# Performance work log

Hardware: AMD Instinct MI355X
Metric: run time of the kernel (lower is better)

Reference implementation:

```python
import jax, jax.numpy as jnp
import numpy as np

B, DV, W, H = 64, 2048, 14, 14
DQ, DA, G, DH, NC = 2400, 1200, 2, 1200, 3000


def setup_inputs() -> dict:
    key = jax.random.key(0)
    ks = jax.random.split(key, 14)
    s = lambda k, shp, scale=0.02: jax.random.normal(k, shp, dtype=jnp.float32) * scale
    return {
        "input_q": jax.random.normal(ks[0], (B, DQ), dtype=jnp.float32),
        "input_v": jax.random.normal(ks[1], (B, DV, W, H), dtype=jnp.float32),
        "Wv_att": s(ks[2], (DA, DV)),
        "bv_att": s(ks[3], (DA,)),
        "Wq_att": s(ks[4], (DA, DQ)),
        "bq_att": s(ks[5], (DA,)),
        "Watt": s(ks[6], (G, DA)),
        "batt": s(ks[7], (G,)),
        "Wv_fus": s(ks[8], (G, DH, DV)),
        "bv_fus": s(ks[9], (G, DH)),
        "Wq_fus": s(ks[10], (G * DH, DQ)),
        "bq_fus": s(ks[11], (G * DH,)),
        "Wc": s(ks[12], (NC, G * DH)),
        "bc": s(ks[13], (NC,)),
    }


def reference(input_q, input_v, Wv_att, bv_att, Wq_att, bq_att, Watt, batt,
              Wv_fus, bv_fus, Wq_fus, bq_fus, Wc, bc):
    b, dv, w, h = input_v.shape
    n = w * h  # spatial positions

    # --- attention branch (eval mode: dropout = identity) ---
    # 1x1 conv == per-position linear over channels; activation_v = tanh
    xv = jnp.tanh(jnp.einsum('bchw,dc->bdhw', input_v, Wv_att) + bv_att[None, :, None, None])
    xv = xv.reshape(b, -1, n).transpose(0, 2, 1)               # [B, WH, DA]
    # question projection; activation_q = tanh
    xq = jnp.tanh(input_q @ Wq_att.T + bq_att)                 # [B, DA]
    # MLB Hadamard fusion + activation_mm = tanh
    xatt = jnp.tanh(xv * xq[:, None, :])                       # [B, WH, DA]
    # glimpse scores: 1x1 conv over dim_mm channels
    wgt = jnp.einsum('bnd,gd->bgn', xatt, Watt) + batt[None, :, None]  # [B, G, WH]
    att = jax.nn.softmax(wgt, axis=-1)                         # softmax over WH per glimpse

    # weighted sum of ORIGINAL features per glimpse
    v_flat = input_v.reshape(b, dv, n)                         # [B, DV, WH]
    v_att = jnp.einsum('bgn,bdn->bgd', att, v_flat)            # [B, G, DV]

    # --- glimpse fusion + classification ---
    v_fus = jnp.tanh(jnp.einsum('bgd,ghd->bgh', v_att, Wv_fus) + bv_fus)  # [B, G, DH]
    v_fus = v_fus.reshape(b, -1)                               # [B, G*DH] (concat over glimpses)
    q_fus = jnp.tanh(input_q @ Wq_fus.T + bq_fus)              # [B, G*DH]
    x = (v_fus * q_fus) @ Wc.T + bc                            # [B, NC]
    return (x, wgt)
```

## Files before the change

kernel.cpp:

```cpp
#include <hip/hip_runtime.h>
#include <hip/hip_fp16.h>

typedef _Float16 half8 __attribute__((ext_vector_type(8)));
typedef float f32x4 __attribute__((ext_vector_type(4)));

__device__ __forceinline__ float tanh_fast(float x) {
  float e = __expf(2.0f * x);
  return 1.0f - 2.0f / (e + 1.0f);
}

__device__ __forceinline__ void gload16(const _Float16* g, _Float16* l) {
  __builtin_amdgcn_global_load_lds((const __attribute__((address_space(1))) void*)g,
                                   (__attribute__((address_space(3))) void*)l,
                                   16, 0, 0);
}

__global__ __launch_bounds__(256) void k_transpose_v(const float* __restrict__ in,
                                                     _Float16* __restrict__ out) {
  __shared__ float t[64][65];
  int b = blockIdx.z;
  int c0 = blockIdx.y * 64;
  int p0 = blockIdx.x * 64;
  int tid = threadIdx.x;
  int pl = tid & 63;
  #pragma unroll
  for (int s = 0; s < 16; ++s) {
    int cl = (tid >> 6) + s * 4;
    int p = p0 + pl;
    t[cl][pl] = (p < 196) ? in[((size_t)b * 2048 + (c0 + cl)) * 196 + p] : 0.0f;
  }
  __syncthreads();
  int c8 = (tid & 7) * 8;
  #pragma unroll
  for (int s = 0; s < 2; ++s) {
    int p = p0 + (tid >> 3) + s * 32;
    if (p < 196) {
      half8 v;
      #pragma unroll
      for (int j = 0; j < 8; ++j) v[j] = (_Float16)t[c8 + j][(tid >> 3) + s * 32];
      *(half8*)(out + ((size_t)b * 196 + p) * 2048 + c0 + c8) = v;
    }
  }
}

__global__ __launch_bounds__(256) void k_prep(const float* __restrict__ W,
                                              _Float16* __restrict__ Wh,
                                              const float* __restrict__ batt,
                                              float* __restrict__ wgt) {
  int i = blockIdx.x * 256 + threadIdx.x;
  int n = i >> 11;
  Wh[i] = (n < 1200) ? (_Float16)W[i] : (_Float16)0.0f;
  if (i < 25088) wgt[i] = batt[(i / 196) & 1];
}

__global__ __launch_bounds__(512, 2) void k_gemm1(const _Float16* __restrict__ A,
                                                  const _Float16* __restrict__ B,
                                                  const float* __restrict__ bias,
                                                  const float* __restrict__ xq,
                                                  const float* __restrict__ Watt,
                                                  float* __restrict__ wgt) {
  __shared__ __align__(16) _Float16 AS[2][256 * 64];
  __shared__ __align__(16) _Float16 BS[2][256 * 64];
  int tid = threadIdx.x;
  int n0 = blockIdx.x * 256;
  int m0 = blockIdx.y * 256;
  int lane = tid & 63;
  int wave = tid >> 6;
  int wm = (wave >> 2) * 128;
  int wn = (wave & 3) * 64;
  int fr = lane & 15;
  int fq = lane >> 4;

  const _Float16* ap[4];
  const _Float16* bp[4];
  int ldso[4];
  #pragma unroll
  for (int i = 0; i < 4; ++i) {
    int g = i * 512 + tid;
    int r = g >> 3, c = g & 7;
    ap[i] = A + (size_t)(m0 + r) * 2048 + ((c ^ (r & 7)) << 3);
    bp[i] = B + (size_t)(n0 + r) * 2048 + ((c ^ (r & 7)) << 3);
    ldso[i] = (i * 512 + (tid & ~63)) << 3;
  }

  f32x4 acc[8][4];
  #pragma unroll
  for (int i = 0; i < 8; ++i)
    #pragma unroll
    for (int j = 0; j < 4; ++j) acc[i][j] = (f32x4){0.f, 0.f, 0.f, 0.f};

  auto stage = [&](int buf, int k0) {
    #pragma unroll
    for (int i = 0; i < 4; ++i) gload16(ap[i] + k0, &AS[buf][ldso[i]]);
    #pragma unroll
    for (int i = 0; i < 4; ++i) gload16(bp[i] + k0, &BS[buf][ldso[i]]);
  };

  auto compute = [&](int buf) {
    half8 a[4][2], b[2][2];
    #pragma unroll
    for (int mh = 0; mh < 2; ++mh) {
      #pragma unroll
      for (int mt = 0; mt < 4; ++mt)
        #pragma unroll
        for (int kk = 0; kk < 2; ++kk) {
          int row = wm + mh * 64 + mt * 16 + fr;
          int c = kk * 4 + fq;
          a[mt][kk] = *(const half8*)(&AS[buf][row * 64 + ((c ^ (row & 7)) << 3)]);
        }
      #pragma unroll
      for (int nh = 0; nh < 2; ++nh) {
        #pragma unroll
        for (int nt = 0; nt < 2; ++nt)
          #pragma unroll
          for (int kk = 0; kk < 2; ++kk) {
            int row = wn + nh * 32 + nt * 16 + fr;
            int c = kk * 4 + fq;
            b[nt][kk] = *(const half8*)(&BS[buf][row * 64 + ((c ^ (row & 7)) << 3)]);
          }
        __builtin_amdgcn_s_setprio(1);
        #pragma unroll
        for (int mt = 0; mt < 4; ++mt)
          #pragma unroll
          for (int nt = 0; nt < 2; ++nt)
            #pragma unroll
            for (int kk = 0; kk < 2; ++kk)
              acc[mh * 4 + mt][nh * 2 + nt] = __builtin_amdgcn_mfma_f32_16x16x32_f16(
                  a[mt][kk], b[nt][kk], acc[mh * 4 + mt][nh * 2 + nt], 0, 0, 0);
        __builtin_amdgcn_s_setprio(0);
      }
    }
  };

  stage(0, 0);
  stage(1, 64);
  for (int t = 0; t < 32; ++t) {
    int cur = t & 1;
    if (t < 31) asm volatile("s_waitcnt vmcnt(8)" ::: "memory");
    else        asm volatile("s_waitcnt vmcnt(0)" ::: "memory");
    __builtin_amdgcn_s_barrier();
    asm volatile("" ::: "memory");
    compute(cur);
    asm volatile("" ::: "memory");
    __builtin_amdgcn_s_barrier();
    if (t < 30) stage(cur, (t + 2) * 64);
  }

  float s0[32], s1[32];
  #pragma unroll
  for (int i = 0; i < 32; ++i) { s0[i] = 0.f; s1[i] = 0.f; }

  #pragma unroll
  for (int nf = 0; nf < 4; ++nf) {
    int col = n0 + wn + (nf >> 1) * 32 + (nf & 1) * 16 + fr;
    bool ok = col < 1200;
    float bcol = ok ? bias[col] : 0.f;
    float wa0 = ok ? Watt[col] : 0.f;
    float wa1 = ok ? Watt[1200 + col] : 0.f;
    int bprev = -1;
    float xqv = 0.f;
    #pragma unroll
    for (int mf = 0; mf < 8; ++mf) {
      #pragma unroll
      for (int r = 0; r < 4; ++r) {
        int row = m0 + wm + (mf >> 2) * 64 + (mf & 3) * 16 + fq * 4 + r;
        int b = row / 196;
        if (b != bprev) { bprev = b; xqv = ok ? xq[b * 1200 + col] : 0.f; }
        float xv = tanh_fast(acc[mf][nf][r] + bcol);
        float xa = tanh_fast(xv * xqv);
        s0[mf * 4 + r] += xa * wa0;
        s1[mf * 4 + r] += xa * wa1;
      }
    }
  }
  #pragma unroll
  for (int i = 0; i < 32; ++i) {
    #pragma unroll
    for (int off = 8; off > 0; off >>= 1) {
      s0[i] += __shfl_down(s0[i], off);
      s1[i] += __shfl_down(s1[i], off);
    }
  }
  if (fr == 0) {
    #pragma unroll
    for (int i = 0; i < 32; ++i) {
      int row = m0 + wm + ((i >> 2) >> 2) * 64 + ((i >> 2) & 3) * 16 + fq * 4 + (i & 3);
      int b = row / 196;
      int p = row - b * 196;
      atomicAdd(&wgt[(b * 2 + 0) * 196 + p], s0[i]);
      atomicAdd(&wgt[(b * 2 + 1) * 196 + p], s1[i]);
    }
  }
}

__global__ __launch_bounds__(256) void k_vatt(const _Float16* __restrict__ Vt,
                                              const float* __restrict__ wgt,
                                              float* __restrict__ v_att) {
  __shared__ float a0s[196], a1s[196];
  int b = blockIdx.y;
  int tid = threadIdx.x;
  int wv = tid >> 6, lane = tid & 63;
  if (wv < 2) {
    const float* wr = wgt + ((size_t)b * 2 + wv) * 196;
    float v[4];
    #pragma unroll
    for (int i = 0; i < 4; ++i) {
      int n = lane + i * 64;
      v[i] = (n < 196) ? wr[n] : -1e30f;
    }
    float mx = fmaxf(fmaxf(v[0], v[1]), fmaxf(v[2], v[3]));
    #pragma unroll
    for (int off = 32; off > 0; off >>= 1) mx = fmaxf(mx, __shfl_xor(mx, off));
    float s = 0.f;
    #pragma unroll
    for (int i = 0; i < 4; ++i) {
      int n = lane + i * 64;
      float e = (n < 196) ? __expf(v[i] - mx) : 0.f;
      v[i] = e;
      s += e;
    }
    #pragma unroll
    for (int off = 32; off > 0; off >>= 1) s += __shfl_xor(s, off);
    float inv = 1.f / s;
    float* dst = wv ? a1s : a0s;
    #pragma unroll
    for (int i = 0; i < 4; ++i) {
      int n = lane + i * 64;
      if (n < 196) dst[n] = v[i] * inv;
    }
  }
  __syncthreads();
  int d = blockIdx.x * 256 + tid;
  const _Float16* vp = Vt + (size_t)b * 196 * 2048 + d;
  float s0 = 0.f, s1 = 0.f;
  for (int n = 0; n < 196; ++n) {
    float v = (float)vp[(size_t)n * 2048];
    s0 += a0s[n] * v;
    s1 += a1s[n] * v;
  }
  v_att[((size_t)b * 2 + 0) * 2048 + d] = s0;
  v_att[((size_t)b * 2 + 1) * 2048 + d] = s1;
}

__global__ __launch_bounds__(256) void k_skinnyQ(const float* __restrict__ q,
                                                 const float* __restrict__ Wa,
                                                 const float* __restrict__ Wf,
                                                 int S, float* __restrict__ P) {
  __shared__ __align__(16) float As[32][64];
  __shared__ __align__(16) float Ws2[32][64];
  int tid = threadIdx.x;
  int x = blockIdx.x;
  int s = blockIdx.y;
  bool f = x >= 19;
  const float* W = f ? Wf : Wa;
  int nt0 = f ? (x - 19) * 64 : x * 64;
  int N = f ? 2400 : 1200;
  int colBase = f ? 1200 : 0;
  const int K = 2400;
  int tiles = K >> 5;
  int t0 = (s * tiles) / S;
  int t1 = ((s + 1) * tiles) / S;
  int tx = tid & 15, ty = tid >> 4;
  int lm = tid >> 2;
  int lk = (tid & 3) * 8;
  const float* Ab = q + (size_t)lm * K;
  int ng = nt0 + lm;
  const float* Wb = W + (size_t)ng * K;
  bool wok = ng < N;
  float acc[4][4] = {};
  for (int t = t0; t < t1; ++t) {
    int k0 = t * 32;
    __syncthreads();
    #pragma unroll
    for (int j = 0; j < 8; ++j) As[lk + j][lm] = Ab[k0 + lk + j];
    #pragma unroll
    for (int j = 0; j < 8; ++j) Ws2[lk + j][lm] = wok ? Wb[k0 + lk + j] : 0.0f;
    __syncthreads();
    #pragma unroll
    for (int kk = 0; kk < 32; ++kk) {
      f32x4 a = *(const f32x4*)&As[kk][ty * 4];
      f32x4 wv = *(const f32x4*)&Ws2[kk][tx * 4];
      #pragma unroll
      for (int i = 0; i < 4; ++i)
        #pragma unroll
        for (int j = 0; j < 4; ++j) acc[i][j] += a[i] * wv[j];
    }
  }
  #pragma unroll
  for (int i = 0; i < 4; ++i) {
    int m = ty * 4 + i;
    #pragma unroll
    for (int j = 0; j < 4; ++j) {
      int nl = nt0 + tx * 4 + j;
      if (nl < N) P[((size_t)s * 64 + m) * 3600 + colBase + nl] = acc[i][j];
    }
  }
}

__global__ __launch_bounds__(256) void k_combineQ(const float* __restrict__ P, int S,
                                                  const float* __restrict__ bq_att,
                                                  const float* __restrict__ bq_fus,
                                                  float* __restrict__ xq,
                                                  float* __restrict__ q_fus) {
  int i = blockIdx.x * 256 + threadIdx.x;
  if (i >= 230400) return;
  int row = i / 3600, col = i % 3600;
  float sum = 0.f;
  for (int ss = 0; ss < S; ++ss) sum += P[(size_t)ss * 230400 + i];
  if (col < 1200) xq[row * 1200 + col] = tanh_fast(sum + bq_att[col]);
  else            q_fus[row * 2400 + col - 1200] = tanh_fast(sum + bq_fus[col - 1200]);
}

__global__ __launch_bounds__(256) void k_skinny(const float* __restrict__ A1,
                                                const float* __restrict__ A2,
                                                int lda, int strideAz,
                                                const float* __restrict__ W, long strideWz,
                                                int N, int K, int S,
                                                float* __restrict__ P, int ldp, int colOffZ) {
  __shared__ __align__(16) float As[32][64];
  __shared__ __align__(16) float Ws2[32][64];
  int tid = threadIdx.x;
  int z = blockIdx.z;
  int s = blockIdx.y;
  int nt0 = blockIdx.x * 64;
  int tiles = K >> 5;
  int t0 = (s * tiles) / S;
  int t1 = ((s + 1) * tiles) / S;
  int tx = tid & 15, ty = tid >> 4;
  int lm = tid >> 2;
  int lk = (tid & 3) * 8;
  const float* Ab = A1 + (size_t)z * strideAz + (size_t)lm * lda;
  const float* A2b = A2 ? (A2 + (size_t)z * strideAz + (size_t)lm * lda) : nullptr;
  int ng = nt0 + lm;
  const float* Wb = W + (size_t)z * strideWz + (size_t)ng * K;
  bool wok = ng < N;
  float acc[4][4] = {};
  for (int t = t0; t < t1; ++t) {
    int k0 = t * 32;
    __syncthreads();
    #pragma unroll
    for (int j = 0; j < 8; ++j) {
      float v = Ab[k0 + lk + j];
      if (A2b) v *= A2b[k0 + lk + j];
      As[lk + j][lm] = v;
    }
    #pragma unroll
    for (int j = 0; j < 8; ++j) Ws2[lk + j][lm] = wok ? Wb[k0 + lk + j] : 0.0f;
    __syncthreads();
    #pragma unroll
    for (int kk = 0; kk < 32; ++kk) {
      f32x4 a = *(const f32x4*)&As[kk][ty * 4];
      f32x4 wv = *(const f32x4*)&Ws2[kk][tx * 4];
      #pragma unroll
      for (int i = 0; i < 4; ++i)
        #pragma unroll
        for (int j = 0; j < 4; ++j) acc[i][j] += a[i] * wv[j];
    }
  }
  #pragma unroll
  for (int i = 0; i < 4; ++i) {
    int m = ty * 4 + i;
    #pragma unroll
    for (int j = 0; j < 4; ++j) {
      int nl = nt0 + tx * 4 + j;
      if (nl < N) P[((size_t)s * 64 + m) * ldp + z * colOffZ + nl] = acc[i][j];
    }
  }
}

__global__ __launch_bounds__(256) void k_combineVh(const float* __restrict__ P, int S,
                                                   const float* __restrict__ bv_fus,
                                                   const float* __restrict__ q_fus,
                                                   float* __restrict__ h) {
  int i = blockIdx.x * 256 + threadIdx.x;
  if (i >= 153600) return;
  int col = i % 2400;
  float sum = bv_fus[col];
  for (int ss = 0; ss < S; ++ss) sum += P[(size_t)ss * 153600 + i];
  h[i] = tanh_fast(sum) * q_fus[i];
}

__global__ __launch_bounds__(256) void k_combine(const float* __restrict__ P, int S, int ldp,
                                                 const float* __restrict__ bias,
                                                 float* __restrict__ out, int total) {
  int i = blockIdx.x * 256 + threadIdx.x;
  if (i >= total) return;
  float sum = bias[i % ldp];
  for (int ss = 0; ss < S; ++ss) sum += P[(size_t)ss * total + i];
  out[i] = sum;
}

extern "C" void kernel_launch(void* const* d_in, const int* in_sizes, int n_in,
                              void* d_out, int out_size, void* d_ws, size_t ws_size,
                              hipStream_t stream) {
  const float* input_q = (const float*)d_in[0];
  const float* input_v = (const float*)d_in[1];
  const float* Wv_att  = (const float*)d_in[2];
  const float* bv_att  = (const float*)d_in[3];
  const float* Wq_att  = (const float*)d_in[4];
  const float* bq_att  = (const float*)d_in[5];
  const float* Watt    = (const float*)d_in[6];
  const float* batt    = (const float*)d_in[7];
  const float* Wv_fus  = (const float*)d_in[8];
  const float* bv_fus  = (const float*)d_in[9];
  const float* Wq_fus  = (const float*)d_in[10];
  const float* bq_fus  = (const float*)d_in[11];
  const float* Wc      = (const float*)d_in[12];
  const float* bc      = (const float*)d_in[13];
  float* out = (float*)d_out;

  char* ws = (char*)d_ws;
  _Float16* Vt   = (_Float16*)ws; ws += 51380224;
  _Float16* Wh   = (_Float16*)ws; ws += 5242880;
  float* xq      = (float*)ws;    ws += 307200;
  float* v_att   = (float*)ws;    ws += 1048576;
  float* v_fus   = (float*)ws;    ws += 614400;
  float* q_fus   = (float*)ws;    ws += 614400;
  float* P       = (float*)ws;    ws += 14745600;

  float* x_out   = out;
  float* wgt_out = out + 192000;

  const int S = 16;

  k_transpose_v<<<dim3(4, 32, 64), dim3(256), 0, stream>>>(input_v, Vt);
  k_prep<<<dim3(10240), dim3(256), 0, stream>>>(Wv_att, Wh, batt, wgt_out);

  k_skinnyQ<<<dim3(57, S), dim3(256), 0, stream>>>(input_q, Wq_att, Wq_fus, S, P);
  k_combineQ<<<dim3(900), dim3(256), 0, stream>>>(P, S, bq_att, bq_fus, xq, q_fus);

  k_gemm1<<<dim3(5, 49), dim3(512), 0, stream>>>(Vt, Wh, bv_att, xq, Watt, wgt_out);

  k_vatt<<<dim3(8, 64), dim3(256), 0, stream>>>(Vt, wgt_out, v_att);

  k_skinny<<<dim3(19, S, 2), dim3(256), 0, stream>>>(v_att, nullptr, 4096, 2048,
                                                     Wv_fus, 1200L * 2048L, 1200, 2048, S, P, 2400, 1200);
  k_combineVh<<<dim3(600), dim3(256), 0, stream>>>(P, S, bv_fus, q_fus, v_fus);

  k_skinny<<<dim3(47, S, 1), dim3(256), 0, stream>>>(v_fus, nullptr, 2400, 0,
                                                     Wc, 0, 3000, 2400, S, P, 3000, 0);
  k_combine<<<dim3(750), dim3(256), 0, stream>>>(P, S, 3000, bc, x_out, 192000);
}
```

Before: 494.1 us.

## Interleave half-tile global-to-LDS loads with MFMA phases in GEMM1 mainloop

```diff
diff --git a/kernel.cpp b/kernel.cpp
--- a/kernel.cpp
+++ b/kernel.cpp
@@ -71,17 +71,22 @@
   int fr = lane & 15;
   int fq = lane >> 4;
 
-  const _Float16* ap[4];
-  const _Float16* bp[4];
-  int ldso[4];
-  #pragma unroll
-  for (int i = 0; i < 4; ++i) {
-    int g = i * 512 + tid;
-    int r = g >> 3, c = g & 7;
-    ap[i] = A + (size_t)(m0 + r) * 2048 + ((c ^ (r & 7)) << 3);
-    bp[i] = B + (size_t)(n0 + r) * 2048 + ((c ^ (r & 7)) << 3);
-    ldso[i] = (i * 512 + (tid & ~63)) << 3;
-  }
+  int lr = lane >> 3;
+  int swz8 = ((lane & 7) ^ lr) << 3;
+  const _Float16* aSrc[2][2];
+  const _Float16* bSrc[2][2];
+  int aDst[2][2], bDst[2][2];
+  #pragma unroll
+  for (int h = 0; h < 2; ++h)
+    #pragma unroll
+    for (int j = 0; j < 2; ++j) {
+      int ra = j * 128 + h * 64 + wave * 8;
+      aSrc[h][j] = A + (size_t)(m0 + ra + lr) * 2048 + swz8;
+      aDst[h][j] = ra * 64;
+      int rb = (j * 2 + (wave >> 2)) * 64 + h * 32 + (wave & 3) * 8;
+      bSrc[h][j] = B + (size_t)(n0 + rb + lr) * 2048 + swz8;
+      bDst[h][j] = rb * 64;
+    }
 
   f32x4 acc[8][4];
   #pragma unroll
@@ -89,106 +94,153 @@
     #pragma unroll
     for (int j = 0; j < 4; ++j) acc[i][j] = (f32x4){0.f, 0.f, 0.f, 0.f};
 
-  auto stage = [&](int buf, int k0) {
-    #pragma unroll
-    for (int i = 0; i < 4; ++i) gload16(ap[i] + k0, &AS[buf][ldso[i]]);
-    #pragma unroll
-    for (int i = 0; i < 4; ++i) gload16(bp[i] + k0, &BS[buf][ldso[i]]);
+  auto stA = [&](int buf, int h, int k0) {
+    gload16(aSrc[h][0] + k0, &AS[buf][aDst[h][0]]);
+    gload16(aSrc[h][1] + k0, &AS[buf][aDst[h][1]]);
   };
-
-  auto compute = [&](int buf) {
-    half8 a[4][2], b[2][2];
-    #pragma unroll
-    for (int mh = 0; mh < 2; ++mh) {
-      #pragma unroll
-      for (int mt = 0; mt < 4; ++mt)
+  auto stB = [&](int buf, int h, int k0) {
+    gload16(bSrc[h][0] + k0, &BS[buf][bDst[h][0]]);
+    gload16(bSrc[h][1] + k0, &BS[buf][bDst[h][1]]);
+  };
+  auto dsA = [&](int buf, int mh, half8 (&a)[4][2]) {
+    #pragma unroll
+    for (int mt = 0; mt < 4; ++mt)
+      #pragma unroll
+      for (int kk = 0; kk < 2; ++kk) {
+        int row = wm + mh * 64 + mt * 16 + fr;
+        int c = kk * 4 + fq;
+        a[mt][kk] = *(const half8*)(&AS[buf][row * 64 + ((c ^ (row & 7)) << 3)]);
+      }
+  };
+  auto dsB = [&](int buf, int nh, half8 (&b)[2][2]) {
+    #pragma unroll
+    for (int nt = 0; nt < 2; ++nt)
+      #pragma unroll
+      for (int kk = 0; kk < 2; ++kk) {
+        int row = wn + nh * 32 + nt * 16 + fr;
+        int c = kk * 4 + fq;
+        b[nt][kk] = *(const half8*)(&BS[buf][row * 64 + ((c ^ (row & 7)) << 3)]);
+      }
+  };
+  auto mma = [&](half8 (&a)[4][2], half8 (&b)[2][2], int mh, int nh) {
+    __builtin_amdgcn_s_setprio(1);
+    #pragma unroll
+    for (int mt = 0; mt < 4; ++mt)
+      #pragma unroll
+      for (int nt = 0; nt < 2; ++nt)
         #pragma unroll
-        for (int kk = 0; kk < 2; ++kk) {
-          int row = wm + mh * 64 + mt * 16 + fr;
-          int c = kk * 4 + fq;
-          a[mt][kk] = *(const half8*)(&AS[buf][row * 64 + ((c ^ (row & 7)) << 3)]);
-        }
-      #pragma unroll
-      for (int nh = 0; nh < 2; ++nh) {
-        #pragma unroll
-        for (int nt = 0; nt < 2; ++nt)
-          #pragma unroll
-          for (int kk = 0; kk < 2; ++kk) {
-            int row = wn + nh * 32 + nt * 16 + fr;
-            int c = kk * 4 + fq;
-            b[nt][kk] = *(const half8*)(&BS[buf][row * 64 + ((c ^ (row & 7)) << 3)]);
-          }
-        __builtin_amdgcn_s_setprio(1);
-        #pragma unroll
-        for (int mt = 0; mt < 4; ++mt)
-          #pragma unroll
-          for (int nt = 0; nt < 2; ++nt)
-            #pragma unroll
-            for (int kk = 0; kk < 2; ++kk)
-              acc[mh * 4 + mt][nh * 2 + nt] = __builtin_amdgcn_mfma_f32_16x16x32_f16(
-                  a[mt][kk], b[nt][kk], acc[mh * 4 + mt][nh * 2 + nt], 0, 0, 0);
-        __builtin_amdgcn_s_setprio(0);
-      }
-    }
+        for (int kk = 0; kk < 2; ++kk)
+          acc[mh * 4 + mt][nh * 2 + nt] = __builtin_amdgcn_mfma_f32_16x16x32_f16(
+              a[mt][kk], b[nt][kk], acc[mh * 4 + mt][nh * 2 + nt], 0, 0, 0);
+    __builtin_amdgcn_s_setprio(0);
   };
 
-  stage(0, 0);
-  stage(1, 64);
-  for (int t = 0; t < 32; ++t) {
-    int cur = t & 1;
-    if (t < 31) asm volatile("s_waitcnt vmcnt(8)" ::: "memory");
-    else        asm volatile("s_waitcnt vmcnt(0)" ::: "memory");
-    __builtin_amdgcn_s_barrier();
-    asm volatile("" ::: "memory");
-    compute(cur);
-    asm volatile("" ::: "memory");
-    __builtin_amdgcn_s_barrier();
-    if (t < 30) stage(cur, (t + 2) * 64);
-  }
-
-  float s0[32], s1[32];
-  #pragma unroll
-  for (int i = 0; i < 32; ++i) { s0[i] = 0.f; s1[i] = 0.f; }
-
+#define BAR() __builtin_amdgcn_s_barrier()
+#define LGKM0() do { asm volatile("s_waitcnt lgkmcnt(0)" ::: "memory"); \
+                     __builtin_amdgcn_sched_barrier(0); } while (0)
+
+  stA(0, 0, 0); stB(0, 0, 0); stB(0, 1, 0); stA(0, 1, 0);
+  stA(1, 0, 64); stB(1, 0, 64); stB(1, 1, 64);
+  asm volatile("s_waitcnt vmcnt(6)" ::: "memory");
+  BAR();
+
+  half8 a[4][2], b0[2][2], b1[2][2];
+  for (int i = 0; i < 16; ++i) {
+    const bool nl = (i < 15);
+    const int kT = i * 128;
+    dsA(0, 0, a); dsB(0, 0, b0);
+    stA(1, 1, kT + 64);
+    BAR(); LGKM0();
+    mma(a, b0, 0, 0);
+    BAR();
+    dsB(0, 1, b1);
+    if (nl) stA(0, 0, kT + 128);
+    BAR(); LGKM0();
+    mma(a, b1, 0, 1);
+    BAR();
+    dsA(0, 1, a);
+    if (nl) stB(0, 0, kT + 128);
+    BAR(); LGKM0();
+    mma(a, b1, 1, 1);
+    BAR();
+    if (nl) {
+      stB(0, 1, kT + 128);
+      asm volatile("s_waitcnt vmcnt(6)" ::: "memory");
+    } else {
+      asm volatile("s_waitcnt vmcnt(0)" ::: "memory");
+    }
+    BAR();
+    mma(a, b0, 1, 0);
+    BAR();
+    dsA(1, 0, a); dsB(1, 0, b0);
+    if (nl) stA(0, 1, kT + 128);
+    BAR(); LGKM0();
+    mma(a, b0, 0, 0);
+    BAR();
+    dsB(1, 1, b1);
+    if (nl) stA(1, 0, kT + 192);
+    BAR(); LGKM0();
+    mma(a, b1, 0, 1);
+    BAR();
+    dsA(1, 1, a);
+    if (nl) stB(1, 0, kT + 192);
+    BAR(); LGKM0();
+    mma(a, b1, 1, 1);
+    BAR();
+    if (nl) {
+      stB(1, 1, kT + 192);
+      asm volatile("s_waitcnt vmcnt(6)" ::: "memory");
+    }
+    BAR();
+    mma(a, b0, 1, 0);
+    BAR();
+  }
+#undef BAR
+#undef LGKM0
+
+  float bcol[4], wa0c[4], wa1c[4], xqv[4];
+  int colv[4]; bool okv[4];
   #pragma unroll
   for (int nf = 0; nf < 4; ++nf) {
     int col = n0 + wn + (nf >> 1) * 32 + (nf & 1) * 16 + fr;
     bool ok = col < 1200;
-    float bcol = ok ? bias[col] : 0.f;
-    float wa0 = ok ? Watt[col] : 0.f;
-    float wa1 = ok ? Watt[1200 + col] : 0.f;
-    int bprev = -1;
-    float xqv = 0.f;
-    #pragma unroll
-    for (int mf = 0; mf < 8; ++mf) {
-      #pragma unroll
-      for (int r = 0; r < 4; ++r) {
-        int row = m0 + wm + (mf >> 2) * 64 + (mf & 3) * 16 + fq * 4 + r;
-        int b = row / 196;
-        if (b != bprev) { bprev = b; xqv = ok ? xq[b * 1200 + col] : 0.f; }
-        float xv = tanh_fast(acc[mf][nf][r] + bcol);
-        float xa = tanh_fast(xv * xqv);
-        s0[mf * 4 + r] += xa * wa0;
-        s1[mf * 4 + r] += xa * wa1;
-      }
-    }
-  }
-  #pragma unroll
-  for (int i = 0; i < 32; ++i) {
-    #pragma unroll
-    for (int off = 8; off > 0; off >>= 1) {
-      s0[i] += __shfl_down(s0[i], off);
-      s1[i] += __shfl_down(s1[i], off);
-    }
-  }
-  if (fr == 0) {
-    #pragma unroll
-    for (int i = 0; i < 32; ++i) {
-      int row = m0 + wm + ((i >> 2) >> 2) * 64 + ((i >> 2) & 3) * 16 + fq * 4 + (i & 3);
+    colv[nf] = col; okv[nf] = ok;
+    bcol[nf] = ok ? bias[col] : 0.f;
+    wa0c[nf] = ok ? Watt[col] : 0.f;
+    wa1c[nf] = ok ? Watt[1200 + col] : 0.f;
+    xqv[nf] = 0.f;
+  }
+  int bprev = -1;
+  #pragma unroll
+  for (int mf = 0; mf < 8; ++mf) {
+    #pragma unroll
+    for (int r = 0; r < 4; ++r) {
+      int row = m0 + wm + (mf >> 2) * 64 + (mf & 3) * 16 + fq * 4 + r;
       int b = row / 196;
-      int p = row - b * 196;
-      atomicAdd(&wgt[(b * 2 + 0) * 196 + p], s0[i]);
-      atomicAdd(&wgt[(b * 2 + 1) * 196 + p], s1[i]);
+      if (b != bprev) {
+        bprev = b;
+        #pragma unroll
+        for (int nf = 0; nf < 4; ++nf)
+          xqv[nf] = okv[nf] ? xq[b * 1200 + colv[nf]] : 0.f;
+      }
+      float t0 = 0.f, t1 = 0.f;
+      #pragma unroll
+      for (int nf = 0; nf < 4; ++nf) {
+        float xv = tanh_fast(acc[mf][nf][r] + bcol[nf]);
+        float xa = tanh_fast(xv * xqv[nf]);
+        t0 += xa * wa0c[nf];
+        t1 += xa * wa1c[nf];
+      }
+      #pragma unroll
+      for (int off = 8; off > 0; off >>= 1) {
+        t0 += __shfl_down(t0, off);
+        t1 += __shfl_down(t1, off);
+      }
+      if (fr == 0) {
+        int p = row - b * 196;
+        atomicAdd(&wgt[(b * 2 + 0) * 196 + p], t0);
+        atomicAdd(&wgt[(b * 2 + 1) * 196 + p], t1);
+      }
     }
   }
 }
```

Result: faster. 443.2 us (-10.3%).
